# Performance work log

Measured on AMD Instinct MI355X. Metric: run time of the kernel, lower is better.

The kernel has to match this reference:

```python
import jax, jax.numpy as jnp
import numpy as np
from jax import lax

B, L, D, K = 4, 4096, 2048, 4
EPS = 1e-5


def setup_inputs() -> dict:
    key = jax.random.key(0)
    k1, k2, k3 = jax.random.split(key, 3)
    x = jax.random.normal(k1, (B, L, D), dtype=jnp.float32)
    # RMSNorm learned scale (torch nn.RMSNorm weight), perturbed around 1
    norm_weight = 1.0 + 0.02 * jax.random.normal(k2, (D,), dtype=jnp.float32)
    # depthwise conv weight in jax 'WIO' layout: (K, 1, D). torch layout is (D, 1, K).
    conv_weight = 0.1 * jax.random.normal(k3, (K, 1, D), dtype=jnp.float32)
    return {"x": x, "norm_weight": norm_weight, "conv_weight": conv_weight}


def reference(x, norm_weight, conv_weight):
    # RMSNorm over last dim: x / sqrt(mean(x^2) + eps) * weight
    ms = jnp.mean(jnp.square(x), axis=-1, keepdims=True)
    x_norm = x * lax.rsqrt(ms + EPS) * norm_weight  # (B, L, D)

    # Depthwise causal conv1d: left-pad K-1 zeros along L (equivalent to
    # torch's symmetric padding=(K-1) followed by [..., :L] slice).
    y = lax.conv_general_dilated(
        x_norm,                     # (B, L, D)
        conv_weight,                # (K, 1, D)
        window_strides=(1,),
        padding=[(K - 1, 0)],
        dimension_numbers=("NWC", "WIO", "NWC"),
        feature_group_count=D,
    )                               # (B, L, D)

    # SiLU activation
    return y * jax.nn.sigmoid(y)
```

## Files before the change

### kernel.cpp

```cpp
#include <hip/hip_runtime.h>

constexpr int B = 4;
constexpr int L = 4096;
constexpr int D = 2048;
constexpr float EPS = 1e-5f;

constexpr int CL = 32;
constexpr int R  = 4;
constexpr int NG = CL / R;
constexpr int NW = 8;
constexpr int NCHUNK = L / CL;
constexpr int NWG = NCHUNK * B;

typedef float floatx4 __attribute__((ext_vector_type(4)));

__device__ __forceinline__ void load4(const float* __restrict__ p, float r[4]) {
    floatx4 v = *reinterpret_cast<const floatx4*>(p);
    r[0] = v.x; r[1] = v.y; r[2] = v.z; r[3] = v.w;
}

__device__ __forceinline__ void light_barrier() {
    asm volatile("s_waitcnt lgkmcnt(0)" ::: "memory");
    __builtin_amdgcn_s_barrier();
    asm volatile("" ::: "memory");
}

__global__ __launch_bounds__(512) void fused_kernel(const float* __restrict__ x,
                                                    const float* __restrict__ nw,
                                                    const float* __restrict__ cw,
                                                    float* __restrict__ out) {
    const int t = threadIdx.x;
    const int wave = t >> 6;
    const int lane = t & 63;

    const int bid = blockIdx.x;
    const int swz = (bid & 7) * (NWG / 8) + (bid >> 3);
    const int b = swz / NCHUNK;
    const int chunk = swz % NCHUNK;
    const int l0 = chunk * CL;
    const int d = t * 4;

    const float* xb = x + (size_t)b * L * D + d;
    float* ob = out + (size_t)b * L * D + d;

    __shared__ float s_red[2][R][NW];

    float nwv[4], wv[4][4];
    load4(nw + d, nwv);
    #pragma unroll
    for (int k = 0; k < 4; ++k) load4(cw + k * D + d, wv[k]);

    float win[3][4];
    {
        float hx[3][4];
        #pragma unroll
        for (int j = 0; j < 3; ++j) {
            const int l = l0 - 3 + j;
            hx[j][0] = hx[j][1] = hx[j][2] = hx[j][3] = 0.0f;
            if (l >= 0) load4(xb + (size_t)l * D, hx[j]);
            float s = hx[j][0]*hx[j][0] + hx[j][1]*hx[j][1]
                    + hx[j][2]*hx[j][2] + hx[j][3]*hx[j][3];
            #pragma unroll
            for (int off = 32; off > 0; off >>= 1)
                s += __shfl_down(s, off, 64);
            if (lane == 0) s_red[0][j][wave] = s;
        }
        light_barrier();
        #pragma unroll
        for (int j = 0; j < 3; ++j) {
            float tot = 0.0f;
            #pragma unroll
            for (int w = 0; w < NW; ++w) tot += s_red[0][j][w];
            float irms = rsqrtf(tot * (1.0f / D) + EPS);
            #pragma unroll
            for (int i = 0; i < 4; ++i) win[j][i] = hx[j][i] * irms * nwv[i];
        }
    }

    float cur[R][4], nxt[R][4];
    #pragma unroll
    for (int r = 0; r < R; ++r)
        load4(xb + (size_t)(l0 + r) * D, cur[r]);

    #pragma unroll
    for (int g = 0; g < NG; ++g) {
        const int par = (g + 1) & 1;

        #pragma unroll
        for (int r = 0; r < R; ++r) {
            float s = cur[r][0]*cur[r][0] + cur[r][1]*cur[r][1]
                    + cur[r][2]*cur[r][2] + cur[r][3]*cur[r][3];
            #pragma unroll
            for (int off = 32; off > 0; off >>= 1)
                s += __shfl_down(s, off, 64);
            if (lane == 0) s_red[par][r][wave] = s;
        }

        if (g + 1 < NG) {
            #pragma unroll
            for (int r = 0; r < R; ++r)
                load4(xb + (size_t)(l0 + (g + 1) * R + r) * D, nxt[r]);
        }

        light_barrier();

        #pragma unroll
        for (int r = 0; r < R; ++r) {
            float tot = 0.0f;
            #pragma unroll
            for (int w = 0; w < NW; ++w) tot += s_red[par][r][w];
            const float irms = rsqrtf(tot * (1.0f / D) + EPS);

            float c[4], y[4];
            #pragma unroll
            for (int i = 0; i < 4; ++i) {
                c[i] = cur[r][i] * irms * nwv[i];
                y[i] = wv[0][i]*win[0][i] + wv[1][i]*win[1][i]
                     + wv[2][i]*win[2][i] + wv[3][i]*c[i];
                y[i] = y[i] / (1.0f + __expf(-y[i]));
            }
            floatx4 o;
            o.x = y[0]; o.y = y[1]; o.z = y[2]; o.w = y[3];
            __builtin_nontemporal_store(o,
                reinterpret_cast<floatx4*>(ob + (size_t)(l0 + g * R + r) * D));

            #pragma unroll
            for (int i = 0; i < 4; ++i) {
                win[0][i] = win[1][i];
                win[1][i] = win[2][i];
                win[2][i] = c[i];
            }
        }

        #pragma unroll
        for (int r = 0; r < R; ++r)
            #pragma unroll
            for (int i = 0; i < 4; ++i) cur[r][i] = nxt[r][i];
    }
}

extern "C" void kernel_launch(void* const* d_in, const int* in_sizes, int n_in,
                              void* d_out, int out_size, void* d_ws, size_t ws_size,
                              hipStream_t stream) {
    const float* x  = (const float*)d_in[0];
    const float* nw = (const float*)d_in[1];
    const float* cw = (const float*)d_in[2];
    float* out = (float*)d_out;

    fused_kernel<<<NWG, 512, 0, stream>>>(x, nw, cw, out);
}
```

Before: 48.86 us.

## Deepen prefetch pipeline to two row groups with triple-buffered reductions

Issues the halo rows and the first two row groups up front, then prefetches two groups ahead inside the loop. Each group's sum-of-squares partials are computed one group early into a triple-buffered shared array, so each iteration's barrier separates writes for group g+1 from reads for group g. The halo reduction is merged into the first barrier. The goal is more memory latency hidden per barrier, at the cost of more registers (an extra 16 floats per thread) and possibly lower occupancy.

New measurement: 47.79 us. -2.2%, faster.

```diff
diff --git a/kernel.cpp b/kernel.cpp
--- a/kernel.cpp
+++ b/kernel.cpp
@@ -43,63 +43,78 @@
     const float* xb = x + (size_t)b * L * D + d;
     float* ob = out + (size_t)b * L * D + d;
 
-    __shared__ float s_red[2][R][NW];
+    __shared__ float s_red[3][R][NW];
+    __shared__ float s_halo[3][NW];
 
     float nwv[4], wv[4][4];
     load4(nw + d, nwv);
     #pragma unroll
     for (int k = 0; k < 4; ++k) load4(cw + k * D + d, wv[k]);
 
-    float win[3][4];
-    {
-        float hx[3][4];
-        #pragma unroll
-        for (int j = 0; j < 3; ++j) {
-            const int l = l0 - 3 + j;
-            hx[j][0] = hx[j][1] = hx[j][2] = hx[j][3] = 0.0f;
-            if (l >= 0) load4(xb + (size_t)l * D, hx[j]);
-            float s = hx[j][0]*hx[j][0] + hx[j][1]*hx[j][1]
-                    + hx[j][2]*hx[j][2] + hx[j][3]*hx[j][3];
-            #pragma unroll
-            for (int off = 32; off > 0; off >>= 1)
-                s += __shfl_down(s, off, 64);
-            if (lane == 0) s_red[0][j][wave] = s;
-        }
-        light_barrier();
-        #pragma unroll
-        for (int j = 0; j < 3; ++j) {
-            float tot = 0.0f;
-            #pragma unroll
-            for (int w = 0; w < NW; ++w) tot += s_red[0][j][w];
-            float irms = rsqrtf(tot * (1.0f / D) + EPS);
-            #pragma unroll
-            for (int i = 0; i < 4; ++i) win[j][i] = hx[j][i] * irms * nwv[i];
-        }
+    float hx[3][4];
+    #pragma unroll
+    for (int j = 0; j < 3; ++j) {
+        const int l = l0 - 3 + j;
+        hx[j][0] = hx[j][1] = hx[j][2] = hx[j][3] = 0.0f;
+        if (l >= 0) load4(xb + (size_t)l * D, hx[j]);
     }
-
-    float cur[R][4], nxt[R][4];
+    float cur[R][4], nxt[R][4], nxt2[R][4];
     #pragma unroll
     for (int r = 0; r < R; ++r)
         load4(xb + (size_t)(l0 + r) * D, cur[r]);
+    #pragma unroll
+    for (int r = 0; r < R; ++r)
+        load4(xb + (size_t)(l0 + R + r) * D, nxt[r]);
+
+    #pragma unroll
+    for (int j = 0; j < 3; ++j) {
+        float s = hx[j][0]*hx[j][0] + hx[j][1]*hx[j][1]
+                + hx[j][2]*hx[j][2] + hx[j][3]*hx[j][3];
+        #pragma unroll
+        for (int off = 32; off > 0; off >>= 1)
+            s += __shfl_down(s, off, 64);
+        if (lane == 0) s_halo[j][wave] = s;
+    }
+    #pragma unroll
+    for (int r = 0; r < R; ++r) {
+        float s = cur[r][0]*cur[r][0] + cur[r][1]*cur[r][1]
+                + cur[r][2]*cur[r][2] + cur[r][3]*cur[r][3];
+        #pragma unroll
+        for (int off = 32; off > 0; off >>= 1)
+            s += __shfl_down(s, off, 64);
+        if (lane == 0) s_red[0][r][wave] = s;
+    }
+    light_barrier();
+
+    float win[3][4];
+    #pragma unroll
+    for (int j = 0; j < 3; ++j) {
+        float tot = 0.0f;
+        #pragma unroll
+        for (int w = 0; w < NW; ++w) tot += s_halo[j][w];
+        float irms = rsqrtf(tot * (1.0f / D) + EPS);
+        #pragma unroll
+        for (int i = 0; i < 4; ++i) win[j][i] = hx[j][i] * irms * nwv[i];
+    }
 
     #pragma unroll
     for (int g = 0; g < NG; ++g) {
-        const int par = (g + 1) & 1;
-
-        #pragma unroll
-        for (int r = 0; r < R; ++r) {
-            float s = cur[r][0]*cur[r][0] + cur[r][1]*cur[r][1]
-                    + cur[r][2]*cur[r][2] + cur[r][3]*cur[r][3];
+        if (g + 1 < NG) {
             #pragma unroll
-            for (int off = 32; off > 0; off >>= 1)
-                s += __shfl_down(s, off, 64);
-            if (lane == 0) s_red[par][r][wave] = s;
+            for (int r = 0; r < R; ++r) {
+                float s = nxt[r][0]*nxt[r][0] + nxt[r][1]*nxt[r][1]
+                        + nxt[r][2]*nxt[r][2] + nxt[r][3]*nxt[r][3];
+                #pragma unroll
+                for (int off = 32; off > 0; off >>= 1)
+                    s += __shfl_down(s, off, 64);
+                if (lane == 0) s_red[(g + 1) % 3][r][wave] = s;
+            }
         }
 
-        if (g + 1 < NG) {
+        if (g + 2 < NG) {
             #pragma unroll
             for (int r = 0; r < R; ++r)
-                load4(xb + (size_t)(l0 + (g + 1) * R + r) * D, nxt[r]);
+                load4(xb + (size_t)(l0 + (g + 2) * R + r) * D, nxt2[r]);
         }
 
         light_barrier();
@@ -108,7 +123,7 @@
         for (int r = 0; r < R; ++r) {
             float tot = 0.0f;
             #pragma unroll
-            for (int w = 0; w < NW; ++w) tot += s_red[par][r][w];
+            for (int w = 0; w < NW; ++w) tot += s_red[g % 3][r][w];
             const float irms = rsqrtf(tot * (1.0f / D) + EPS);
 
             float c[4], y[4];
@@ -135,7 +150,10 @@
         #pragma unroll
         for (int r = 0; r < R; ++r)
             #pragma unroll
-            for (int i = 0; i < 4; ++i) cur[r][i] = nxt[r][i];
+            for (int i = 0; i < 4; ++i) {
+                cur[r][i] = nxt[r][i];
+                nxt[r][i] = nxt2[r][i];
+            }
     }
 }
 
```
